# Optimization experiments

Hardware: AMD Instinct MI355X
Metric: run time of the kernel (lower is better)

## Reference

```python
import jax, jax.numpy as jnp
import numpy as np

N_NODES = 200000
N_HYPEREDGES = 50000
NNZ = 3200000
D = 128
LEAKY = 0.2


def setup_inputs() -> dict:
    key = jax.random.key(0)
    k1, k2, k3, k4 = jax.random.split(key, 4)
    embs = jax.random.normal(k1, (N_NODES, D), dtype=jnp.float32)
    vals = jax.random.uniform(k2, (NNZ,), dtype=jnp.float32)
    rows = jax.random.randint(k3, (NNZ,), 0, N_NODES, dtype=jnp.int32)
    cols = jax.random.randint(k4, (NNZ,), 0, N_HYPEREDGES, dtype=jnp.int32)
    return {
        "embs": embs,
        "vals": vals,
        "rows": rows,
        "cols": cols,
        "n_nodes": N_NODES,
        "n_hyperedges": N_HYPEREDGES,
    }


def reference(embs, vals, rows, cols, n_nodes, n_hyperedges):
    # adj is sparse COO: adj[rows[k], cols[k]] = vals[k], shape [n_nodes, n_hyperedges]
    # Step 1: he = adj.T @ embs  -> [n_hyperedges, D]
    he = jax.ops.segment_sum(embs[rows] * vals[:, None], cols,
                             num_segments=n_hyperedges)
    # Step 2: out = adj @ he     -> [n_nodes, D]
    out = jax.ops.segment_sum(he[cols] * vals[:, None], rows,
                              num_segments=n_nodes)
    # LeakyReLU(negative_slope=LEAKY)
    return jnp.where(out >= 0, out, LEAKY * out)
```

## Files before the change

kernel.cpp:

```cpp
#include <hip/hip_runtime.h>

#define DIM 128
#define LEAKY 0.2f
#define N_NODES_C 200000
#define N_HE_C 50000

#define SLAB2 11008
#define NB 782
#define SEGC_PB 64
#define SEGR_PB 256
#define CAP_B 4608

typedef float f32x4 __attribute__((ext_vector_type(4)));

__device__ __forceinline__ unsigned bf16r(float f) {
    return (__float_as_uint(f) + 0x8000u) >> 16;
}
__device__ __forceinline__ float bf16lo(unsigned u) {
    return __uint_as_float((u & 0xFFFFu) << 16);
}
__device__ __forceinline__ float bf16hi(unsigned u) {
    return __uint_as_float(u & 0xFFFF0000u);
}

__global__ void convert_bf16(const f32x4* __restrict__ in, uint2* __restrict__ out, int n4) {
    int t = blockIdx.x * blockDim.x + threadIdx.x;
    if (t >= n4) return;
    f32x4 x = __builtin_nontemporal_load(in + t);
    out[t] = make_uint2((bf16r(x.y) << 16) | bf16r(x.x),
                        (bf16r(x.w) << 16) | bf16r(x.z));
}

template <int MODE>
__global__ void __launch_bounds__(512)
bin_side(const int* __restrict__ rows, const int* __restrict__ cols,
         const float* __restrict__ vals, int nnz,
         int* __restrict__ cur, int2* __restrict__ stag) {
    __shared__ int2 sorted[SLAB2];
    __shared__ unsigned short bkt[SLAB2];
    __shared__ int cnt[NB];
    __shared__ int scn[NB];
    __shared__ int gb[NB];
    __shared__ int part[512];
    int t = threadIdx.x;
    int base = blockIdx.x * SLAB2;
    int nloc = nnz - base; if (nloc > SLAB2) nloc = SLAB2;
    if (nloc < 0) nloc = 0;
    for (int i = t; i < NB; i += 512) cnt[i] = 0;
    __syncthreads();
    for (int i = t; i < nloc; i += 512) {
        int key = (MODE == 0) ? (cols[base + i] >> 6) : (rows[base + i] >> 8);
        atomicAdd(&cnt[key], 1);
    }
    __syncthreads();
    int c0 = (2 * t     < NB) ? cnt[2 * t]     : 0;
    int c1 = (2 * t + 1 < NB) ? cnt[2 * t + 1] : 0;
    part[t] = c0 + c1;
    __syncthreads();
    for (int off = 1; off < 512; off <<= 1) {
        int x = part[t];
        int add = (t >= off) ? part[t - off] : 0;
        __syncthreads();
        part[t] = x + add;
        __syncthreads();
    }
    int pex = t ? part[t - 1] : 0;
    if (2 * t < NB) {
        scn[2 * t] = pex;
        gb[2 * t] = c0 ? atomicAdd(&cur[2 * t], c0) : 0;
    }
    if (2 * t + 1 < NB) {
        scn[2 * t + 1] = pex + c0;
        gb[2 * t + 1] = c1 ? atomicAdd(&cur[2 * t + 1], c1) : 0;
    }
    __syncthreads();
    for (int i = t; i < NB; i += 512) cnt[i] = scn[i];
    __syncthreads();
    for (int i = t; i < nloc; i += 512) {
        int k = base + i;
        int r = rows[k], c = cols[k];
        int v = __float_as_int(vals[k]);
        int key, x;
        if (MODE == 0) { key = c >> 6; x = ((c & 63) << 18) | r; }
        else           { key = r >> 8; x = ((r & 255) << 16) | c; }
        int p = atomicAdd(&cnt[key], 1);
        sorted[p] = make_int2(x, v);
        bkt[p] = (unsigned short)key;
    }
    __syncthreads();
    for (int i = t; i < nloc; i += 512) {
        int b = bkt[i];
        int off = gb[b] + (i - scn[b]);
        if (off < CAP_B)
            stag[(size_t)b * CAP_B + off] = sorted[i];
    }
}

template <int SEG_PB, int LSHIFT, int MODE>
__global__ void __launch_bounds__(256)
bucket_sort(const int* __restrict__ cur, const int2* __restrict__ stag,
            unsigned* __restrict__ outPacked,
            int* __restrict__ startOut, int* __restrict__ endOut, int nseg) {
    __shared__ int2 ent[CAP_B];
    __shared__ int cnt[SEG_PB];
    __shared__ int scn[SEG_PB];
    int b = blockIdx.x;
    size_t lo = (size_t)b * CAP_B;
    int n = cur[b]; if (n > CAP_B) n = CAP_B;
    int t = threadIdx.x;
    for (int i = t; i < SEG_PB; i += 256) cnt[i] = 0;
    __syncthreads();
    for (int i = t; i < n; i += 256) {
        int2 e = stag[lo + i];
        ent[i] = e;
        atomicAdd(&cnt[e.x >> LSHIFT], 1);
    }
    __syncthreads();
    if (t < SEG_PB) scn[t] = cnt[t];
    __syncthreads();
    for (int off = 1; off < SEG_PB; off <<= 1) {
        int x = (t < SEG_PB) ? scn[t] : 0;
        int add = (t >= off && t < SEG_PB) ? scn[t - off] : 0;
        __syncthreads();
        if (t < SEG_PB) scn[t] = x + add;
        __syncthreads();
    }
    int segBase = b * SEG_PB;
    if (t < SEG_PB) {
        int excl = t ? scn[t - 1] : 0;
        if (segBase + t < nseg) {
            startOut[segBase + t] = (int)lo + excl;
            endOut[segBase + t]   = (int)lo + scn[t];
        }
        cnt[t] = excl;
    }
    __syncthreads();
    for (int i = t; i < n; i += 256) {
        int2 e = ent[i];
        int s = e.x >> LSHIFT;
        int pos = (int)lo + atomicAdd(&cnt[s], 1);
        unsigned w;
        if (MODE == 0) {
            unsigned v14 = ((unsigned)e.y + 0x10000u) >> 17;
            w = ((unsigned)(e.x & 0x3FFFF) << 14) | (v14 & 0x3FFFu);
        } else {
            unsigned vb = ((unsigned)e.y + 0x8000u) >> 16;
            w = ((unsigned)(e.x & 0xFFFF) << 16) | vb;
        }
        outPacked[pos] = w;
    }
}


__global__ void seg_pass1(const int* __restrict__ start, const int* __restrict__ end,
                          const unsigned* __restrict__ packed,
                          const uint2* __restrict__ srcb2, uint2* __restrict__ dstb2,
                          int nseg) {
    int wid = (int)((blockIdx.x * (unsigned)blockDim.x + threadIdx.x) >> 6);
    int lane = threadIdx.x & 63;
    if (wid >= nseg) return;
    int g = lane >> 5;
    int l = lane & 31;
    int s = start[wid];
    int e = end[wid];
    int mid = s + ((e - s) >> 1);
    int js = g ? mid : s;
    int je = g ? e : mid;
    float a0 = 0.f, a1 = 0.f, a2 = 0.f, a3 = 0.f;
    int j = js;
    for (; j + 8 <= je; j += 8) {
        #pragma unroll
        for (int u = 0; u < 8; ++u) {
            unsigned p = packed[j + u];
            uint2 w = srcb2[(size_t)(p >> 14) * 32 + l];
            float v = __uint_as_float((p & 0x3FFFu) << 17);
            a0 += bf16lo(w.x) * v; a1 += bf16hi(w.x) * v;
            a2 += bf16lo(w.y) * v; a3 += bf16hi(w.y) * v;
        }
    }
    for (; j < je; ++j) {
        unsigned p = packed[j];
        uint2 w = srcb2[(size_t)(p >> 14) * 32 + l];
        float v = __uint_as_float((p & 0x3FFFu) << 17);
        a0 += bf16lo(w.x) * v; a1 += bf16hi(w.x) * v;
        a2 += bf16lo(w.y) * v; a3 += bf16hi(w.y) * v;
    }
    a0 += __shfl_xor(a0, 32, 64);
    a1 += __shfl_xor(a1, 32, 64);
    a2 += __shfl_xor(a2, 32, 64);
    a3 += __shfl_xor(a3, 32, 64);
    if (g == 0) {
        uint2 o;
        o.x = (bf16r(a1) << 16) | bf16r(a0);
        o.y = (bf16r(a3) << 16) | bf16r(a2);
        dstb2[(size_t)wid * 32 + l] = o;
    }
}

__global__ void seg_pass2(const int* __restrict__ start, const int* __restrict__ end,
                          const unsigned* __restrict__ packed,
                          const uint2* __restrict__ srcb2, float* __restrict__ dst,
                          int nseg) {
    int wid = (int)((blockIdx.x * (unsigned)blockDim.x + threadIdx.x) >> 6);
    int lane = threadIdx.x & 63;
    if (wid >= nseg) return;
    int g = lane >> 5;
    int l = lane & 31;
    int s = start[wid];
    int e = end[wid];
    int mid = s + ((e - s) >> 1);
    int js = g ? mid : s;
    int je = g ? e : mid;
    float a0 = 0.f, a1 = 0.f, a2 = 0.f, a3 = 0.f;
    int j = js;
    for (; j + 4 <= je; j += 4) {
        #pragma unroll
        for (int u = 0; u < 4; ++u) {
            unsigned p = packed[j + u];
            uint2 w = srcb2[(size_t)(p >> 16) * 32 + l];
            float v = __uint_as_float(p << 16);
            a0 += bf16lo(w.x) * v; a1 += bf16hi(w.x) * v;
            a2 += bf16lo(w.y) * v; a3 += bf16hi(w.y) * v;
        }
    }
    for (; j < je; ++j) {
        unsigned p = packed[j];
        uint2 w = srcb2[(size_t)(p >> 16) * 32 + l];
        float v = __uint_as_float(p << 16);
        a0 += bf16lo(w.x) * v; a1 += bf16hi(w.x) * v;
        a2 += bf16lo(w.y) * v; a3 += bf16hi(w.y) * v;
    }
    a0 += __shfl_xor(a0, 32, 64);
    a1 += __shfl_xor(a1, 32, 64);
    a2 += __shfl_xor(a2, 32, 64);
    a3 += __shfl_xor(a3, 32, 64);
    if (g == 0) {
        a0 = a0 >= 0.f ? a0 : LEAKY * a0;
        a1 = a1 >= 0.f ? a1 : LEAKY * a1;
        a2 = a2 >= 0.f ? a2 : LEAKY * a2;
        a3 = a3 >= 0.f ? a3 : LEAKY * a3;
        f32x4 o = {a0, a1, a2, a3};
        __builtin_nontemporal_store(o,
            reinterpret_cast<f32x4*>(dst) + (size_t)wid * 32 + l);
    }
}

__global__ void scatter_step(const float* __restrict__ src, const float* __restrict__ vals,
                             const int* __restrict__ gidx, const int* __restrict__ sidx,
                             float* __restrict__ dst, int nnz) {
    long long t = (long long)blockIdx.x * blockDim.x + threadIdx.x;
    int k = (int)(t >> 5);
    if (k >= nnz) return;
    int q = ((int)t & 31) << 2;
    int g = gidx[k];
    int s = sidx[k];
    float v = vals[k];
    const float4 e = *reinterpret_cast<const float4*>(src + (size_t)g * DIM + q);
    float* dp = dst + (size_t)s * DIM + q;
    unsafeAtomicAdd(dp + 0, e.x * v);
    unsafeAtomicAdd(dp + 1, e.y * v);
    unsafeAtomicAdd(dp + 2, e.z * v);
    unsafeAtomicAdd(dp + 3, e.w * v);
}

__global__ void leaky_inplace(float* __restrict__ out, int n4) {
    int t = blockIdx.x * blockDim.x + threadIdx.x;
    if (t >= n4) return;
    float4* p = reinterpret_cast<float4*>(out) + t;
    float4 x = *p;
    x.x = x.x >= 0.f ? x.x : LEAKY * x.x;
    x.y = x.y >= 0.f ? x.y : LEAKY * x.y;
    x.z = x.z >= 0.f ? x.z : LEAKY * x.z;
    x.w = x.w >= 0.f ? x.w : LEAKY * x.w;
    *p = x;
}

extern "C" void kernel_launch(void* const* d_in, const int* in_sizes, int n_in,
                              void* d_out, int out_size, void* d_ws, size_t ws_size,
                              hipStream_t stream) {
    const float* embs = (const float*)d_in[0];
    const float* vals = (const float*)d_in[1];
    const int*   rows = (const int*)d_in[2];
    const int*   cols = (const int*)d_in[3];
    const int nnz = in_sizes[1];
    float* out = (float*)d_out;

    unsigned* embsB = (unsigned*)d_out;

    char* ws = (char*)d_ws;
    size_t off = 0;
    auto alloc = [&](size_t bytes) -> char* {
        char* p = ws + off;
        off = (off + bytes + 255) & ~(size_t)255;
        return p;
    };
    unsigned* heB   = (unsigned*)alloc((size_t)N_HE_C * DIM * 2);
    int* startC     = (int*)alloc((size_t)N_HE_C * sizeof(int));
    int* endC       = (int*)alloc((size_t)N_HE_C * sizeof(int));
    int* startR     = (int*)alloc((size_t)N_NODES_C * sizeof(int));
    int* endR       = (int*)alloc((size_t)N_NODES_C * sizeof(int));
    int* curC       = (int*)alloc((size_t)NB * sizeof(int));
    int* curR       = (int*)alloc((size_t)NB * sizeof(int));
    int2* stagC     = (int2*)alloc((size_t)NB * CAP_B * sizeof(int2));
    int2* stagR     = (int2*)alloc((size_t)NB * CAP_B * sizeof(int2));
    size_t required = off;

    if (ws_size < required) {
        float* he = (float*)d_ws;
        (void)hipMemsetAsync(he,  0, (size_t)N_HE_C * DIM * sizeof(float), stream);
        (void)hipMemsetAsync(out, 0, (size_t)N_NODES_C * DIM * sizeof(float), stream);
        long long nthreads = (long long)nnz * 32;
        dim3 grd((unsigned)((nthreads + 255) / 256));
        scatter_step<<<grd, 256, 0, stream>>>(embs, vals, rows, cols, he, nnz);
        scatter_step<<<grd, 256, 0, stream>>>(he, vals, cols, rows, out, nnz);
        int n4 = N_NODES_C * DIM / 4;
        leaky_inplace<<<(n4 + 255) / 256, 256, 0, stream>>>(out, n4);
        return;
    }

    (void)hipMemsetAsync(curC, 0, (size_t)NB * sizeof(int), stream);
    (void)hipMemsetAsync(curR, 0, (size_t)NB * sizeof(int), stream);

    int nslab = (nnz + SLAB2 - 1) / SLAB2;
    bin_side<0><<<nslab, 512, 0, stream>>>(rows, cols, vals, nnz, curC, stagC);
    bin_side<1><<<nslab, 512, 0, stream>>>(rows, cols, vals, nnz, curR, stagR);

    bucket_sort<SEGC_PB, 18, 0><<<NB, 256, 0, stream>>>(
        curC, stagC, (unsigned*)stagC, startC, endC, N_HE_C);
    bucket_sort<SEGR_PB, 16, 1><<<NB, 256, 0, stream>>>(
        curR, stagR, (unsigned*)stagR, startR, endR, N_NODES_C);

    {
        int n4 = N_NODES_C * DIM / 4;
        convert_bf16<<<(n4 + 255) / 256, 256, 0, stream>>>(
            (const f32x4*)embs, (uint2*)embsB, n4);
    }

    seg_pass1<<<(N_HE_C + 3) / 4, 256, 0, stream>>>(
        startC, endC, (const unsigned*)stagC, (const uint2*)embsB, (uint2*)heB, N_HE_C);
    seg_pass2<<<(N_NODES_C + 3) / 4, 256, 0, stream>>>(
        startR, endR, (const unsigned*)stagR, (const uint2*)heB, out, N_NODES_C);
}
```

Before: 402.2 us.

## Fuse bucket sort into segment gather kernels using shared-memory sorted keys

Replaces the separate bucket_sort and seg_pass kernels with fused kernels that count, scan and sort each bucket's entries into shared memory, then immediately perform the per-segment weighted gathers from that shared buffer. This removes the global writes and reads of packed sorted keys and the start/end index arrays, plus two kernel launches. In exchange, each 1024-thread block processes many segments serially per wave, so there is less parallelism and latency hiding for the random gathers, and there is a risk of tail imbalance across only 782 blocks.

```diff
diff --git a/kernel.cpp b/kernel.cpp
--- a/kernel.cpp
+++ b/kernel.cpp
@@ -96,152 +96,166 @@
     }
 }
 
-template <int SEG_PB, int LSHIFT, int MODE>
-__global__ void __launch_bounds__(256)
-bucket_sort(const int* __restrict__ cur, const int2* __restrict__ stag,
-            unsigned* __restrict__ outPacked,
-            int* __restrict__ startOut, int* __restrict__ endOut, int nseg) {
-    __shared__ int2 ent[CAP_B];
-    __shared__ int cnt[SEG_PB];
-    __shared__ int scn[SEG_PB];
+
+__global__ void __launch_bounds__(1024)
+bucket_gather1(const int* __restrict__ cur, const int2* __restrict__ stag,
+               const uint2* __restrict__ srcb2, uint2* __restrict__ dstb2,
+               int nhe) {
+    __shared__ unsigned key4[CAP_B];
+    __shared__ int cnt[SEGC_PB];
+    __shared__ int scn[SEGC_PB];
     int b = blockIdx.x;
     size_t lo = (size_t)b * CAP_B;
     int n = cur[b]; if (n > CAP_B) n = CAP_B;
     int t = threadIdx.x;
-    for (int i = t; i < SEG_PB; i += 256) cnt[i] = 0;
-    __syncthreads();
-    for (int i = t; i < n; i += 256) {
+    if (t < SEGC_PB) cnt[t] = 0;
+    __syncthreads();
+    for (int i = t; i < n; i += 1024)
+        atomicAdd(&cnt[stag[lo + i].x >> 18], 1);
+    __syncthreads();
+    if (t < SEGC_PB) scn[t] = cnt[t];
+    __syncthreads();
+    for (int off = 1; off < SEGC_PB; off <<= 1) {
+        int x = (t < SEGC_PB) ? scn[t] : 0;
+        int add = (t >= off && t < SEGC_PB) ? scn[t - off] : 0;
+        __syncthreads();
+        if (t < SEGC_PB) scn[t] = x + add;
+        __syncthreads();
+    }
+    if (t < SEGC_PB) cnt[t] = t ? scn[t - 1] : 0;
+    __syncthreads();
+    for (int i = t; i < n; i += 1024) {
         int2 e = stag[lo + i];
-        ent[i] = e;
-        atomicAdd(&cnt[e.x >> LSHIFT], 1);
-    }
-    __syncthreads();
-    if (t < SEG_PB) scn[t] = cnt[t];
-    __syncthreads();
-    for (int off = 1; off < SEG_PB; off <<= 1) {
-        int x = (t < SEG_PB) ? scn[t] : 0;
-        int add = (t >= off && t < SEG_PB) ? scn[t - off] : 0;
-        __syncthreads();
-        if (t < SEG_PB) scn[t] = x + add;
-        __syncthreads();
-    }
-    int segBase = b * SEG_PB;
-    if (t < SEG_PB) {
-        int excl = t ? scn[t - 1] : 0;
-        if (segBase + t < nseg) {
-            startOut[segBase + t] = (int)lo + excl;
-            endOut[segBase + t]   = (int)lo + scn[t];
-        }
-        cnt[t] = excl;
-    }
-    __syncthreads();
-    for (int i = t; i < n; i += 256) {
-        int2 e = ent[i];
-        int s = e.x >> LSHIFT;
-        int pos = (int)lo + atomicAdd(&cnt[s], 1);
-        unsigned w;
-        if (MODE == 0) {
-            unsigned v14 = ((unsigned)e.y + 0x10000u) >> 17;
-            w = ((unsigned)(e.x & 0x3FFFF) << 14) | (v14 & 0x3FFFu);
-        } else {
-            unsigned vb = ((unsigned)e.y + 0x8000u) >> 16;
-            w = ((unsigned)(e.x & 0xFFFF) << 16) | vb;
-        }
-        outPacked[pos] = w;
-    }
-}
-
-
-__global__ void seg_pass1(const int* __restrict__ start, const int* __restrict__ end,
-                          const unsigned* __restrict__ packed,
-                          const uint2* __restrict__ srcb2, uint2* __restrict__ dstb2,
-                          int nseg) {
-    int wid = (int)((blockIdx.x * (unsigned)blockDim.x + threadIdx.x) >> 6);
-    int lane = threadIdx.x & 63;
-    if (wid >= nseg) return;
-    int g = lane >> 5;
-    int l = lane & 31;
-    int s = start[wid];
-    int e = end[wid];
-    int mid = s + ((e - s) >> 1);
-    int js = g ? mid : s;
-    int je = g ? e : mid;
-    float a0 = 0.f, a1 = 0.f, a2 = 0.f, a3 = 0.f;
-    int j = js;
-    for (; j + 8 <= je; j += 8) {
-        #pragma unroll
-        for (int u = 0; u < 8; ++u) {
-            unsigned p = packed[j + u];
+        int seg = e.x >> 18;
+        unsigned v14 = ((unsigned)e.y + 0x10000u) >> 17;
+        unsigned w = ((unsigned)(e.x & 0x3FFFF) << 14) | (v14 & 0x3FFFu);
+        key4[atomicAdd(&cnt[seg], 1)] = w;
+    }
+    __syncthreads();
+    int wv = t >> 6;
+    int lane = t & 63;
+    int g = lane >> 5, l = lane & 31;
+    #pragma unroll
+    for (int ss = 0; ss < 4; ++ss) {
+        int seg = wv * 4 + ss;
+        int he = b * SEGC_PB + seg;
+        if (he >= nhe) continue;
+        int s = seg ? scn[seg - 1] : 0;
+        int e = scn[seg];
+        int mid = s + ((e - s) >> 1);
+        int js = g ? mid : s;
+        int je = g ? e : mid;
+        float a0 = 0.f, a1 = 0.f, a2 = 0.f, a3 = 0.f;
+        int j = js;
+        for (; j + 8 <= je; j += 8) {
+            #pragma unroll
+            for (int u = 0; u < 8; ++u) {
+                unsigned p = key4[j + u];
+                uint2 w = srcb2[(size_t)(p >> 14) * 32 + l];
+                float v = __uint_as_float((p & 0x3FFFu) << 17);
+                a0 += bf16lo(w.x) * v; a1 += bf16hi(w.x) * v;
+                a2 += bf16lo(w.y) * v; a3 += bf16hi(w.y) * v;
+            }
+        }
+        for (; j < je; ++j) {
+            unsigned p = key4[j];
             uint2 w = srcb2[(size_t)(p >> 14) * 32 + l];
             float v = __uint_as_float((p & 0x3FFFu) << 17);
             a0 += bf16lo(w.x) * v; a1 += bf16hi(w.x) * v;
             a2 += bf16lo(w.y) * v; a3 += bf16hi(w.y) * v;
         }
-    }
-    for (; j < je; ++j) {
-        unsigned p = packed[j];
-        uint2 w = srcb2[(size_t)(p >> 14) * 32 + l];
-        float v = __uint_as_float((p & 0x3FFFu) << 17);
-        a0 += bf16lo(w.x) * v; a1 += bf16hi(w.x) * v;
-        a2 += bf16lo(w.y) * v; a3 += bf16hi(w.y) * v;
-    }
-    a0 += __shfl_xor(a0, 32, 64);
-    a1 += __shfl_xor(a1, 32, 64);
-    a2 += __shfl_xor(a2, 32, 64);
-    a3 += __shfl_xor(a3, 32, 64);
-    if (g == 0) {
-        uint2 o;
-        o.x = (bf16r(a1) << 16) | bf16r(a0);
-        o.y = (bf16r(a3) << 16) | bf16r(a2);
-        dstb2[(size_t)wid * 32 + l] = o;
-    }
-}
-
-__global__ void seg_pass2(const int* __restrict__ start, const int* __restrict__ end,
-                          const unsigned* __restrict__ packed,
-                          const uint2* __restrict__ srcb2, float* __restrict__ dst,
-                          int nseg) {
-    int wid = (int)((blockIdx.x * (unsigned)blockDim.x + threadIdx.x) >> 6);
-    int lane = threadIdx.x & 63;
-    if (wid >= nseg) return;
-    int g = lane >> 5;
-    int l = lane & 31;
-    int s = start[wid];
-    int e = end[wid];
-    int mid = s + ((e - s) >> 1);
-    int js = g ? mid : s;
-    int je = g ? e : mid;
-    float a0 = 0.f, a1 = 0.f, a2 = 0.f, a3 = 0.f;
-    int j = js;
-    for (; j + 4 <= je; j += 4) {
-        #pragma unroll
-        for (int u = 0; u < 4; ++u) {
-            unsigned p = packed[j + u];
+        a0 += __shfl_xor(a0, 32, 64);
+        a1 += __shfl_xor(a1, 32, 64);
+        a2 += __shfl_xor(a2, 32, 64);
+        a3 += __shfl_xor(a3, 32, 64);
+        if (g == 0) {
+            uint2 o;
+            o.x = (bf16r(a1) << 16) | bf16r(a0);
+            o.y = (bf16r(a3) << 16) | bf16r(a2);
+            dstb2[(size_t)he * 32 + l] = o;
+        }
+    }
+}
+
+__global__ void __launch_bounds__(1024)
+bucket_gather2(const int* __restrict__ cur, const int2* __restrict__ stag,
+               const uint2* __restrict__ srcb2, float* __restrict__ dst,
+               int nn) {
+    __shared__ unsigned key4[CAP_B];
+    __shared__ int cnt[SEGR_PB];
+    __shared__ int scn[SEGR_PB];
+    int b = blockIdx.x;
+    size_t lo = (size_t)b * CAP_B;
+    int n = cur[b]; if (n > CAP_B) n = CAP_B;
+    int t = threadIdx.x;
+    if (t < SEGR_PB) cnt[t] = 0;
+    __syncthreads();
+    for (int i = t; i < n; i += 1024)
+        atomicAdd(&cnt[(stag[lo + i].x >> 16) & 255], 1);
+    __syncthreads();
+    if (t < SEGR_PB) scn[t] = cnt[t];
+    __syncthreads();
+    for (int off = 1; off < SEGR_PB; off <<= 1) {
+        int x = (t < SEGR_PB) ? scn[t] : 0;
+        int add = (t >= off && t < SEGR_PB) ? scn[t - off] : 0;
+        __syncthreads();
+        if (t < SEGR_PB) scn[t] = x + add;
+        __syncthreads();
+    }
+    if (t < SEGR_PB) cnt[t] = t ? scn[t - 1] : 0;
+    __syncthreads();
+    for (int i = t; i < n; i += 1024) {
+        int2 e = stag[lo + i];
+        int seg = (e.x >> 16) & 255;
+        unsigned vb = ((unsigned)e.y + 0x8000u) >> 16;
+        unsigned w = ((unsigned)(e.x & 0xFFFF) << 16) | vb;
+        key4[atomicAdd(&cnt[seg], 1)] = w;
+    }
+    __syncthreads();
+    int wv = t >> 6;
+    int lane = t & 63;
+    int g = lane >> 5, l = lane & 31;
+    for (int ss = 0; ss < 16; ++ss) {
+        int seg = wv * 16 + ss;
+        int node = b * SEGR_PB + seg;
+        if (node >= nn) continue;
+        int s = seg ? scn[seg - 1] : 0;
+        int e = scn[seg];
+        int mid = s + ((e - s) >> 1);
+        int js = g ? mid : s;
+        int je = g ? e : mid;
+        float a0 = 0.f, a1 = 0.f, a2 = 0.f, a3 = 0.f;
+        int j = js;
+        for (; j + 4 <= je; j += 4) {
+            #pragma unroll
+            for (int u = 0; u < 4; ++u) {
+                unsigned p = key4[j + u];
+                uint2 w = srcb2[(size_t)(p >> 16) * 32 + l];
+                float v = __uint_as_float(p << 16);
+                a0 += bf16lo(w.x) * v; a1 += bf16hi(w.x) * v;
+                a2 += bf16lo(w.y) * v; a3 += bf16hi(w.y) * v;
+            }
+        }
+        for (; j < je; ++j) {
+            unsigned p = key4[j];
             uint2 w = srcb2[(size_t)(p >> 16) * 32 + l];
             float v = __uint_as_float(p << 16);
             a0 += bf16lo(w.x) * v; a1 += bf16hi(w.x) * v;
             a2 += bf16lo(w.y) * v; a3 += bf16hi(w.y) * v;
         }
-    }
-    for (; j < je; ++j) {
-        unsigned p = packed[j];
-        uint2 w = srcb2[(size_t)(p >> 16) * 32 + l];
-        float v = __uint_as_float(p << 16);
-        a0 += bf16lo(w.x) * v; a1 += bf16hi(w.x) * v;
-        a2 += bf16lo(w.y) * v; a3 += bf16hi(w.y) * v;
-    }
-    a0 += __shfl_xor(a0, 32, 64);
-    a1 += __shfl_xor(a1, 32, 64);
-    a2 += __shfl_xor(a2, 32, 64);
-    a3 += __shfl_xor(a3, 32, 64);
-    if (g == 0) {
-        a0 = a0 >= 0.f ? a0 : LEAKY * a0;
-        a1 = a1 >= 0.f ? a1 : LEAKY * a1;
-        a2 = a2 >= 0.f ? a2 : LEAKY * a2;
-        a3 = a3 >= 0.f ? a3 : LEAKY * a3;
-        f32x4 o = {a0, a1, a2, a3};
-        __builtin_nontemporal_store(o,
-            reinterpret_cast<f32x4*>(dst) + (size_t)wid * 32 + l);
+        a0 += __shfl_xor(a0, 32, 64);
+        a1 += __shfl_xor(a1, 32, 64);
+        a2 += __shfl_xor(a2, 32, 64);
+        a3 += __shfl_xor(a3, 32, 64);
+        if (g == 0) {
+            a0 = a0 >= 0.f ? a0 : LEAKY * a0;
+            a1 = a1 >= 0.f ? a1 : LEAKY * a1;
+            a2 = a2 >= 0.f ? a2 : LEAKY * a2;
+            a3 = a3 >= 0.f ? a3 : LEAKY * a3;
+            f32x4 o = {a0, a1, a2, a3};
+            __builtin_nontemporal_store(o,
+                reinterpret_cast<f32x4*>(dst) + (size_t)node * 32 + l);
+        }
     }
 }
 
@@ -295,10 +309,6 @@
         return p;
     };
     unsigned* heB   = (unsigned*)alloc((size_t)N_HE_C * DIM * 2);
-    int* startC     = (int*)alloc((size_t)N_HE_C * sizeof(int));
-    int* endC       = (int*)alloc((size_t)N_HE_C * sizeof(int));
-    int* startR     = (int*)alloc((size_t)N_NODES_C * sizeof(int));
-    int* endR       = (int*)alloc((size_t)N_NODES_C * sizeof(int));
     int* curC       = (int*)alloc((size_t)NB * sizeof(int));
     int* curR       = (int*)alloc((size_t)NB * sizeof(int));
     int2* stagC     = (int2*)alloc((size_t)NB * CAP_B * sizeof(int2));
@@ -325,19 +335,14 @@
     bin_side<0><<<nslab, 512, 0, stream>>>(rows, cols, vals, nnz, curC, stagC);
     bin_side<1><<<nslab, 512, 0, stream>>>(rows, cols, vals, nnz, curR, stagR);
 
-    bucket_sort<SEGC_PB, 18, 0><<<NB, 256, 0, stream>>>(
-        curC, stagC, (unsigned*)stagC, startC, endC, N_HE_C);
-    bucket_sort<SEGR_PB, 16, 1><<<NB, 256, 0, stream>>>(
-        curR, stagR, (unsigned*)stagR, startR, endR, N_NODES_C);
-
     {
         int n4 = N_NODES_C * DIM / 4;
         convert_bf16<<<(n4 + 255) / 256, 256, 0, stream>>>(
             (const f32x4*)embs, (uint2*)embsB, n4);
     }
 
-    seg_pass1<<<(N_HE_C + 3) / 4, 256, 0, stream>>>(
-        startC, endC, (const unsigned*)stagC, (const uint2*)embsB, (uint2*)heB, N_HE_C);
-    seg_pass2<<<(N_NODES_C + 3) / 4, 256, 0, stream>>>(
-        startR, endR, (const unsigned*)stagR, (const uint2*)heB, out, N_NODES_C);
-}
+    bucket_gather1<<<NB, 1024, 0, stream>>>(
+        curC, stagC, (const uint2*)embsB, (uint2*)heB, N_HE_C);
+    bucket_gather2<<<NB, 1024, 0, stream>>>(
+        curR, stagR, (const uint2*)heB, out, N_NODES_C);
+}
```

Result: faster. 371.4 us (-7.7%).
